# Optimization experiments

Hardware: AMD Instinct MI355X
Metric: run time of the kernel (lower is better)

Reference implementation:

```python
import jax, jax.numpy as jnp
import numpy as np

B, T, I, H = 512, 64, 128, 128
E = I - 1  # encoder_in


def _cell(x, h, c, Wih, Whh, bih, bhh):
    # PyTorch LSTM gate order: i, f, g, o
    g = x @ Wih.T + h @ Whh.T + bih + bhh
    i, f, gg, o = jnp.split(g, 4, axis=-1)
    c2 = jax.nn.sigmoid(f) * c + jax.nn.sigmoid(i) * jnp.tanh(gg)
    h2 = jax.nn.sigmoid(o) * jnp.tanh(c2)
    return h2, c2


def setup_inputs() -> dict:
    key = jax.random.key(0)
    ks = iter(jax.random.split(key, 40))
    n = lambda *s: jax.random.normal(next(ks), s, dtype=jnp.float32) * 0.05
    inp = {
        'input_data': jax.random.normal(next(ks), (B, T, I), dtype=jnp.float32),
        # encoder LSTM (2 layers, input E)
        'enc_Wih0': n(4 * H, E), 'enc_Whh0': n(4 * H, H), 'enc_bih0': n(4 * H), 'enc_bhh0': n(4 * H),
        'enc_Wih1': n(4 * H, H), 'enc_Whh1': n(4 * H, H), 'enc_bih1': n(4 * H), 'enc_bhh1': n(4 * H),
        # decoder LSTM (2 layers, input 1)
        'dec_Wih0': n(4 * H, 1), 'dec_Whh0': n(4 * H, H), 'dec_bih0': n(4 * H), 'dec_bhh0': n(4 * H),
        'dec_Wih1': n(4 * H, H), 'dec_Whh1': n(4 * H, H), 'dec_bih1': n(4 * H), 'dec_bhh1': n(4 * H),
        # input attention MLP: (2H+T)->T->1
        'attn_W1': n(T, 2 * H + T), 'attn_b1': n(T), 'attn_W2': n(1, T), 'attn_b2': n(1),
        # temporal attention MLP: 3H->H->1
        'attnd_W1': n(H, 3 * H), 'attnd_b1': n(H), 'attnd_W2': n(1, H), 'attnd_b2': n(1),
        # decoder input projection (H+1)->1 and output projection 2H->1
        'decin_W': n(1, H + 1), 'decin_b': n(1),
        'proj_W': n(1, 2 * H), 'proj_b': n(1),
    }
    return inp


def reference(input_data, enc_Wih0, enc_Whh0, enc_bih0, enc_bhh0,
              enc_Wih1, enc_Whh1, enc_bih1, enc_bhh1,
              dec_Wih0, dec_Whh0, dec_bih0, dec_bhh0,
              dec_Wih1, dec_Whh1, dec_bih1, dec_bhh1,
              attn_W1, attn_b1, attn_W2, attn_b2,
              attnd_W1, attnd_b1, attnd_W2, attnd_b2,
              decin_W, decin_b, proj_W, proj_b):
    b, t, i = input_data.shape
    e, hdim = i - 1, enc_Whh0.shape[1]
    inp_enc = input_data[:, :, 1:]              # [B,T,E]
    inp_dec = input_data[:, :, 0]               # [B,T]
    inp_perm = jnp.transpose(inp_enc, (0, 2, 1))  # [B,E,T]
    z = jnp.zeros((b, hdim), input_data.dtype)

    def enc_step(carry, x_t):
        h0, c0, h1, c1 = carry
        hc = jnp.concatenate([
            jnp.broadcast_to(h1[:, None, :], (b, e, hdim)),
            jnp.broadcast_to(c1[:, None, :], (b, e, hdim)),
            inp_perm], axis=-1)                              # [B,E,2H+T]
        logits = jnp.tanh(hc @ attn_W1.T + attn_b1) @ attn_W2.T + attn_b2
        a = jax.nn.softmax(logits[..., 0], axis=-1)          # [B,E]
        h0, c0 = _cell(x_t * a, h0, c0, enc_Wih0, enc_Whh0, enc_bih0, enc_bhh0)
        h1, c1 = _cell(h0, h1, c1, enc_Wih1, enc_Whh1, enc_bih1, enc_bhh1)
        return (h0, c0, h1, c1), h1

    _, h_top = jax.lax.scan(enc_step, (z, z, z, z), jnp.transpose(inp_enc, (1, 0, 2)))
    h_exp = jnp.transpose(h_top, (1, 0, 2))  # [B,T,H]

    def dec_step(carry, x_t):
        h0, c0, h1, c1, _ = carry
        hc = jnp.concatenate([
            jnp.broadcast_to(h1[:, None, :], (b, t, hdim)),
            jnp.broadcast_to(c1[:, None, :], (b, t, hdim)),
            h_exp], axis=-1)                                  # [B,T,3H]
        logits = jnp.tanh(hc @ attnd_W1.T + attnd_b1) @ attnd_W2.T + attnd_b2
        a = jax.nn.softmax(logits[..., 0], axis=-1)           # [B,T]
        partial = jnp.einsum('bth,bt->bh', h_exp, a)          # [B,H]
        full = jnp.concatenate([partial, x_t[:, None]], axis=-1)  # [B,H+1]
        din = full @ decin_W.T + decin_b                      # [B,1]
        h0, c0 = _cell(din, h0, c0, dec_Wih0, dec_Whh0, dec_bih0, dec_bhh0)
        h1, c1 = _cell(h0, h1, c1, dec_Wih1, dec_Whh1, dec_bih1, dec_bhh1)
        return (h0, c0, h1, c1, partial), None

    (h0, c0, h1, c1, partial), _ = jax.lax.scan(dec_step, (z, z, z, z, z), jnp.transpose(inp_dec))
    out = jnp.concatenate([h1, partial], axis=-1) @ proj_W.T + proj_b  # [B,1]
    return out
```

## Files before the change

kernel.cpp:

```cpp
#include <hip/hip_runtime.h>

#define BATCH 512
#define TT 64
#define II 128

#define OFF_Wr_e0 0
#define OFF_Wr_e1 (OFF_Wr_e0 + 512*256)
#define OFF_Wr_d1 (OFF_Wr_e1 + 512*256)
#define OFF_bs0e  (OFF_Wr_d1 + 512*256)
#define OFF_bs1e  (OFF_bs0e + 512)
#define OFF_bs0d  (OFF_bs1e + 512)
#define OFF_bs1d  (OFF_bs0d + 512)
#define OFF_xprojT (OFF_bs1d + 512)
#define OFF_hexp   (OFF_xprojT + BATCH*8192)
#define OFF_hprojT (OFF_hexp + BATCH*8192)

struct Params {
  const float* input;
  const float *eWih0, *eWhh0, *ebih0, *ebhh0, *eWih1, *eWhh1, *ebih1, *ebhh1;
  const float *dWih0, *dWhh0, *dbih0, *dbhh0, *dWih1, *dWhh1, *dbih1, *dbhh1;
  const float *aW1, *ab1, *aW2, *ab2;
  const float *adW1, *adb1, *adW2, *adb2;
  const float *dinW, *dinb, *projW, *projb;
  float* ws;
  float* out;
};

#define L2E 1.4426950408889634f

__device__ __forceinline__ float exp2f_(float x){ return __builtin_amdgcn_exp2f(x); }
__device__ __forceinline__ float rcp_(float x){ return __builtin_amdgcn_rcpf(x); }
__device__ __forceinline__ float fast_tanh(float x){
  float t = exp2f_(x * 2.8853900817779268f);
  return 1.f - 2.f * rcp_(t + 1.f);
}
__device__ __forceinline__ float sigm(float x){
  return rcp_(1.f + exp2f_(-x * L2E));
}
__device__ __forceinline__ float wave_max(float v){
  #pragma unroll
  for (int o = 32; o > 0; o >>= 1) v = fmaxf(v, __shfl_xor(v, o, 64));
  return v;
}
__device__ __forceinline__ float wave_sum(float v){
  #pragma unroll
  for (int o = 32; o > 0; o >>= 1) v += __shfl_xor(v, o, 64);
  return v;
}
__device__ __forceinline__ void bar_lds(){
  asm volatile("s_waitcnt lgkmcnt(0)\n\ts_barrier" ::: "memory");
}

#define FMA4(W,V0,V1,V2,V3) \
  a0 += (W).x*(V0).x + (W).y*(V0).y + (W).z*(V0).z + (W).w*(V0).w; \
  a1 += (W).x*(V1).x + (W).y*(V1).y + (W).z*(V1).z + (W).w*(V1).w; \
  a2 += (W).x*(V2).x + (W).y*(V2).y + (W).z*(V2).z + (W).w*(V2).w; \
  a3 += (W).x*(V3).x + (W).y*(V3).y + (W).z*(V3).z + (W).w*(V3).w;

__global__ __launch_bounds__(256) void k_prep(Params p){
  float* ws = p.ws;
  const int gid = blockIdx.x*256 + threadIdx.x;
  const int gsz = gridDim.x*256;
  for (int i = gid; i < 512*256; i += gsz){
    const int j = i >> 8, k = i & 255;
    ws[OFF_Wr_e0 + i] = (k < 128) ? ((k < 127) ? p.eWih0[j*127 + k] : 0.f)
                                  : p.eWhh0[j*128 + (k-128)];
    ws[OFF_Wr_e1 + i] = (k < 128) ? p.eWih1[j*128 + k] : p.eWhh1[j*128 + (k-128)];
    ws[OFF_Wr_d1 + i] = (k < 128) ? p.dWih1[j*128 + k] : p.dWhh1[j*128 + (k-128)];
  }
  for (int i = gid; i < 512; i += gsz){
    ws[OFF_bs0e+i] = p.ebih0[i]+p.ebhh0[i];
    ws[OFF_bs1e+i] = p.ebih1[i]+p.ebhh1[i];
    ws[OFF_bs0d+i] = p.dbih0[i]+p.dbhh0[i];
    ws[OFF_bs1d+i] = p.dbih1[i]+p.dbhh1[i];
  }
}

__global__ __launch_bounds__(256) void k_xproj(Params p){
  __shared__ float xin[64][128];
  __shared__ float w1x[64][64];
  __shared__ float b1s[64];
  const int b = blockIdx.x, tid = threadIdx.x;
  const float* inb = p.input + (size_t)b*(TT*II);
  for (int i = tid; i < 64*128; i += 256){
    const int k = i >> 7, e = i & 127;
    xin[k][e] = (e < 127) ? inb[k*II + 1 + e] : 0.f;
  }
  for (int i = tid; i < 64*64; i += 256){
    const int j = i >> 6, k = i & 63;
    w1x[j][k] = p.aW1[j*320 + 256 + k];
  }
  if (tid < 64) b1s[tid] = p.ab1[tid];
  __syncthreads();
  float* outb = p.ws + OFF_xprojT + (size_t)b*8192;
  for (int i = tid; i < 64*128; i += 256){
    const int j = i >> 7, e = i & 127;
    float acc = b1s[j];
    #pragma unroll 8
    for (int k = 0; k < 64; ++k) acc += xin[k][e] * w1x[j][k];
    outb[i] = acc;
  }
}

__global__ __launch_bounds__(256) void k_hproj(Params p){
  __shared__ float hx[64][129];
  __shared__ float bs[128];
  const int b = blockIdx.x, tid = threadIdx.x;
  const float* hb = p.ws + OFF_hexp + (size_t)b*8192;
  for (int i = tid; i < 64*128; i += 256) hx[i>>7][i&127] = hb[i];
  if (tid < 128) bs[tid] = p.adb1[tid];
  __syncthreads();
  float* outb = p.ws + OFF_hprojT + (size_t)b*8192;
  for (int i = tid; i < 128*64; i += 256){
    const int kk = i >> 6, t2 = i & 63;
    const float* w = p.adW1 + kk*384 + 256;
    float acc = bs[kk];
    #pragma unroll 8
    for (int k = 0; k < 128; ++k) acc += hx[t2][k] * w[k];
    outb[i] = acc;
  }
}

#define ENC_LDS_FLOATS 39776
__global__ __launch_bounds__(1024, 4) void k_enc(Params p){
  extern __shared__ float sm[];
  float* xp   = sm;
  float* Se   = xp + 32768;
  float* c0s  = Se + 2048;
  float* gpA  = c0s + 512;
  float* gpB  = gpA + 2048;
  float* g01s = gpB + 2048;
  float* w2   = g01s + 256;
  float* pm   = w2 + 64;
  float* psu  = pm + 16;
  const int tid = threadIdx.x;
  const int b0 = blockIdx.x*4;
  float* ws = p.ws;

  { const float4* xsrc = (const float4*)(ws + OFF_xprojT + (size_t)b0*8192);
    float4* xdst = (float4*)xp;
    for (int i = tid; i < 8192; i += 1024) xdst[i] = xsrc[i]; }
  for (int i = tid; i < 2048; i += 1024) Se[i] = 0.f;
  if (tid < 512) c0s[tid] = 0.f;
  if (tid < 64) w2[tid] = p.aW2[tid];
  const float b2 = p.ab2[0];

  const int bbW = tid >> 8;
  const int wvq = (tid >> 6) & 3;
  const int kqE = tid & 3, oE = tid >> 2, jjE = oE & 63;
  const int jhE = tid & 1, eE = (tid >> 1) & 127;
  const int jG = tid & 511, khG = tid >> 9;
  const float bias0 = ws[OFF_bs0e + jG];
  const float bias1 = ws[OFF_bs1e + jG];
  const float4* wE1 = (const float4*)(p.aW1 + jjE*320 + kqE*64);
  const float4* wE3 = (const float4*)(ws + OFF_Wr_e0 + (jG<<8) + (khG<<7));
  const float4* wE4 = (const float4*)(ws + OFF_Wr_e1 + (jG<<8) + (khG<<7));
  const float* xrow = p.input + (size_t)(b0+bbW)*8192 + 1 + eE;
  float4 pfE1[4], pfE3[4], pfE4[4];
  #pragma unroll
  for (int i = 0; i < 4; ++i){ pfE1[i]=wE1[i]; pfE3[i]=wE3[i]; pfE4[i]=wE4[i]; }
  __syncthreads();

  for (int t = 0; t < TT; ++t){
    {
      const float4* s1 = (const float4*)(Se + bbW*512 + 256 + kqE*64);
      float a = 0.f;
      #pragma unroll
      for (int kg = 0; kg < 4; ++kg){ float4 w = pfE1[kg], x = s1[kg];
        a += w.x*x.x + w.y*x.y + w.z*x.z + w.w*x.w; }
      #pragma unroll
      for (int kg = 4; kg < 16; ++kg){ float4 w = wE1[kg], x = s1[kg];
        a += w.x*x.x + w.y*x.y + w.z*x.z + w.w*x.w; }
      a += __shfl_xor(a, 1, 64);
      a += __shfl_xor(a, 2, 64);
      if (kqE == 0) g01s[oE] = a;
    }
    bar_lds();
    float accL;
    {
      const float* xpe = xp + bbW*8192 + eE;
      const float* gg = g01s + bbW*64 + jhE*32;
      const float* w2p = w2 + jhE*32;
      float a = 0.f;
      #pragma unroll 8
      for (int q = 0; q < 32; ++q)
        a += w2p[q] * fast_tanh(xpe[(jhE*32+q)*128] + gg[q]);
      a += __shfl_xor(a, 1, 64);
      a += b2;
      if (eE == 127) a = -3.0e38f;
      accL = a;
      const float m = wave_max(a);
      const float pe = exp2f_((a - m)*L2E);
      const float s = wave_sum(pe)*0.5f;
      if ((tid & 63) == 0){ pm[bbW*4+wvq] = m; psu[bbW*4+wvq] = s; }
    }
    bar_lds();
    {
      const float m0=pm[bbW*4],m1=pm[bbW*4+1],m2=pm[bbW*4+2],m3=pm[bbW*4+3];
      const float gm = fmaxf(fmaxf(m0,m1),fmaxf(m2,m3));
      const float tot = psu[bbW*4]*exp2f_((m0-gm)*L2E) + psu[bbW*4+1]*exp2f_((m1-gm)*L2E)
                      + psu[bbW*4+2]*exp2f_((m2-gm)*L2E) + psu[bbW*4+3]*exp2f_((m3-gm)*L2E);
      const float a = exp2f_((accL-gm)*L2E)*rcp_(tot);
      float xv = 0.f;
      if (eE < 127) xv = xrow[t*128] * a;
      Se[bbW*512 + eE] = xv;
    }
    bar_lds();
    {
      float a0,a1,a2,a3; a0=a1=a2=a3 = khG ? 0.f : bias0;
      const float4* x0 = (const float4*)(Se + (khG<<7));
      const float4* x1 = x0 + 128; const float4* x2 = x0 + 256; const float4* x3 = x0 + 384;
      #pragma unroll
      for (int kg = 0; kg < 4; ++kg){ float4 w = pfE3[kg];
        float4 v0=x0[kg],v1=x1[kg],v2=x2[kg],v3=x3[kg]; FMA4(w,v0,v1,v2,v3) }
      #pragma unroll 7
      for (int kg = 4; kg < 32; ++kg){ float4 w = wE3[kg];
        float4 v0=x0[kg],v1=x1[kg],v2=x2[kg],v3=x3[kg]; FMA4(w,v0,v1,v2,v3) }
      float* gp = khG ? gpB : gpA;
      gp[jG]=a0; gp[512+jG]=a1; gp[1024+jG]=a2; gp[1536+jG]=a3;
    }
    bar_lds();
    if (tid < 512){
      const int bb = tid>>7, u = tid&127;
      const float* gA = gpA + bb*512; const float* gB = gpB + bb*512;
      const float gi=gA[u]+gB[u], gf=gA[128+u]+gB[128+u];
      const float gg2=gA[256+u]+gB[256+u], go=gA[384+u]+gB[384+u];
      const float c = sigm(gf)*c0s[tid] + sigm(gi)*fast_tanh(gg2);
      c0s[tid] = c;
      Se[bb*512 + 128 + u] = sigm(go)*fast_tanh(c);
    }
    bar_lds();
    {
      float a0,a1,a2,a3; a0=a1=a2=a3 = khG ? 0.f : bias1;
      const float4* x0 = (const float4*)(Se + 128 + (khG<<7));
      const float4* x1 = x0 + 128; const float4* x2 = x0 + 256; const float4* x3 = x0 + 384;
      #pragma unroll
      for (int kg = 0; kg < 4; ++kg){ float4 w = pfE4[kg];
        float4 v0=x0[kg],v1=x1[kg],v2=x2[kg],v3=x3[kg]; FMA4(w,v0,v1,v2,v3) }
      #pragma unroll 7
      for (int kg = 4; kg < 32; ++kg){ float4 w = wE4[kg];
        float4 v0=x0[kg],v1=x1[kg],v2=x2[kg],v3=x3[kg]; FMA4(w,v0,v1,v2,v3) }
      float* gp = khG ? gpB : gpA;
      gp[jG]=a0; gp[512+jG]=a1; gp[1024+jG]=a2; gp[1536+jG]=a3;
    }
    bar_lds();
    if (tid < 512){
      const int bb = tid>>7, u = tid&127;
      const float* gA = gpA + bb*512; const float* gB = gpB + bb*512;
      const float gi=gA[u]+gB[u], gf=gA[128+u]+gB[128+u];
      const float gg2=gA[256+u]+gB[256+u], go=gA[384+u]+gB[384+u];
      const float c = sigm(gf)*Se[bb*512+384+u] + sigm(gi)*fast_tanh(gg2);
      Se[bb*512+384+u] = c;
      const float h = sigm(go)*fast_tanh(c);
      Se[bb*512+256+u] = h;
      __builtin_nontemporal_store(h, ws + OFF_hexp + (size_t)(b0+bb)*8192 + t*128 + u);
    }
    bar_lds();
  }
}

#define DEC_LDS_FLOATS 40880
__global__ __launch_bounds__(1024, 4) void k_dec(Params p){
  extern __shared__ float sm[];
  float* hp    = sm;
  float* Sd    = hp + 33280;
  float* c0s   = Sd + 1536;
  float* gpA   = c0s + 512;
  float* gpB   = gpA + 2048;
  float* parts = gpB + 2048;
  float* g01d  = parts + 512;
  float* lraw  = g01d + 512;
  float* pm    = lraw + 256;
  float* psu   = pm + 16;
  float* dpart = psu + 16;
  float* wd2   = dpart + 16;
  const int tid = threadIdx.x;
  const int b0 = blockIdx.x*4;
  float* ws = p.ws;

  { const float* hsrc = ws + OFF_hprojT + (size_t)b0*8192;
    for (int i = tid; i < 32768; i += 1024){
      const int bb = i>>13, kk = (i>>6)&127, tl = i&63;
      hp[bb*8320 + kk*65 + tl] = hsrc[i];
    } }
  for (int i = tid; i < 1536; i += 1024) Sd[i] = 0.f;
  if (tid < 512) c0s[tid] = 0.f;
  if (tid < 128) wd2[tid] = p.adW2[tid];
  const float bd2 = p.adb2[0];

  const int bbW = tid >> 8, wvq = (tid >> 6) & 3;
  const int khD = tid & 1, kkD = (tid >> 1) & 127;
  const int kq4 = tid & 3, o4 = tid >> 2, tl4 = o4 & 63;
  const int thC = tid & 1, hC = (tid >> 1) & 127;
  const int jG = tid & 511, khG = tid >> 9;
  const float bias0d = ws[OFF_bs0d + jG];
  const float bias1d = ws[OFF_bs1d + jG];
  const float dW0j = p.dWih0[jG];
  const float dinw_h = p.dinW[hC];
  const float dinw128 = p.dinW[128], dinbv = p.dinb[0];
  const float4* wD1 = (const float4*)(p.adW1 + kkD*384 + khD*128);
  const float4* wD3 = (const float4*)(p.dWhh0 + (jG<<7) + (khG<<6));
  const float4* wD4 = (const float4*)(ws + OFF_Wr_d1 + (jG<<8) + (khG<<7));
  const float* heB = ws + OFF_hexp + (size_t)(b0+bbW)*8192 + thC*4096 + hC;
  float4 pfD1[4], pfD3[4], pfD4[4];
  #pragma unroll
  for (int i = 0; i < 4; ++i){ pfD1[i]=wD1[i]; pfD3[i]=wD3[i]; pfD4[i]=wD4[i]; }
  __syncthreads();

  for (int t = 0; t < TT; ++t){
    {
      const float4* sx = (const float4*)(Sd + bbW*384 + 128 + khD*128);
      float a = 0.f;
      #pragma unroll
      for (int kg = 0; kg < 4; ++kg){ float4 w = pfD1[kg], x = sx[kg];
        a += w.x*x.x + w.y*x.y + w.z*x.z + w.w*x.w; }
      #pragma unroll 7
      for (int kg = 4; kg < 32; ++kg){ float4 w = wD1[kg], x = sx[kg];
        a += w.x*x.x + w.y*x.y + w.z*x.z + w.w*x.w; }
      a += __shfl_xor(a, 1, 64);
      if (khD == 0) g01d[bbW*128 + kkD] = a;
    }
    bar_lds();
    float lacc;
    {
      const float* hpb = hp + bbW*8320 + tl4;
      const float* gg = g01d + bbW*128;
      float a = 0.f;
      #pragma unroll 8
      for (int q = 0; q < 32; ++q){
        const int kk = q*4 + kq4;
        a += wd2[kk] * fast_tanh(hpb[kk*65] + gg[kk]);
      }
      a += __shfl_xor(a, 1, 64);
      a += __shfl_xor(a, 2, 64);
      a += bd2;
      lacc = a;
      if (kq4 == 0) lraw[o4] = a;
      const float m = wave_max(a);
      const float pe = exp2f_((a-m)*L2E);
      const float s = wave_sum(pe)*0.25f;
      if ((tid&63)==0){ pm[bbW*4+wvq]=m; psu[bbW*4+wvq]=s; }
    }
    bar_lds();
    if (tid < 256){
      const int bb = tid>>6;
      const float m0=pm[bb*4],m1=pm[bb*4+1],m2=pm[bb*4+2],m3=pm[bb*4+3];
      const float gm = fmaxf(fmaxf(m0,m1),fmaxf(m2,m3));
      const float tot = psu[bb*4]*exp2f_((m0-gm)*L2E)+psu[bb*4+1]*exp2f_((m1-gm)*L2E)
                      +psu[bb*4+2]*exp2f_((m2-gm)*L2E)+psu[bb*4+3]*exp2f_((m3-gm)*L2E);
      lraw[tid] = exp2f_((lraw[tid]-gm)*L2E)*rcp_(tot);
    }
    bar_lds();
    {
      const float* av = lraw + bbW*64 + thC*32;
      float a = 0.f;
      #pragma unroll 8
      for (int q = 0; q < 32; ++q) a += av[q] * heB[q*128];
      a += __shfl_xor(a, 1, 64);
      if (thC == 0) parts[bbW*128 + hC] = a;
      float v = a * dinw_h;
      v = wave_sum(v)*0.5f;
      if ((tid&63)==0) dpart[bbW*4+wvq] = v;
    }
    bar_lds();
    {
      const float xd0 = p.input[(size_t)(b0+0)*8192 + t*128];
      const float xd1 = p.input[(size_t)(b0+1)*8192 + t*128];
      const float xd2 = p.input[(size_t)(b0+2)*8192 + t*128];
      const float xd3 = p.input[(size_t)(b0+3)*8192 + t*128];
      const float dn0 = dpart[0]+dpart[1]+dpart[2]+dpart[3] + xd0*dinw128 + dinbv;
      const float dn1 = dpart[4]+dpart[5]+dpart[6]+dpart[7] + xd1*dinw128 + dinbv;
      const float dn2 = dpart[8]+dpart[9]+dpart[10]+dpart[11] + xd2*dinw128 + dinbv;
      const float dn3 = dpart[12]+dpart[13]+dpart[14]+dpart[15] + xd3*dinw128 + dinbv;
      float a0,a1,a2,a3;
      if (khG){ a0=a1=a2=a3=0.f; }
      else { a0=bias0d+dn0*dW0j; a1=bias0d+dn1*dW0j; a2=bias0d+dn2*dW0j; a3=bias0d+dn3*dW0j; }
      const float4* x0 = (const float4*)(Sd + (khG<<6));
      const float4* x1 = x0 + 96; const float4* x2 = x0 + 192; const float4* x3 = x0 + 288;
      #pragma unroll
      for (int kg = 0; kg < 4; ++kg){ float4 w = pfD3[kg];
        float4 v0=x0[kg],v1=x1[kg],v2=x2[kg],v3=x3[kg]; FMA4(w,v0,v1,v2,v3) }
      #pragma unroll
      for (int kg = 4; kg < 16; ++kg){ float4 w = wD3[kg];
        float4 v0=x0[kg],v1=x1[kg],v2=x2[kg],v3=x3[kg]; FMA4(w,v0,v1,v2,v3) }
      float* gp = khG ? gpB : gpA;
      gp[jG]=a0; gp[512+jG]=a1; gp[1024+jG]=a2; gp[1536+jG]=a3;
    }
    bar_lds();
    if (tid < 512){
      const int bb = tid>>7, u = tid&127;
      const float* gA = gpA + bb*512; const float* gB = gpB + bb*512;
      const float gi=gA[u]+gB[u], gf=gA[128+u]+gB[128+u];
      const float gg2=gA[256+u]+gB[256+u], go=gA[384+u]+gB[384+u];
      const float c = sigm(gf)*c0s[tid] + sigm(gi)*fast_tanh(gg2);
      c0s[tid] = c;
      Sd[bb*384 + u] = sigm(go)*fast_tanh(c);
    }
    bar_lds();
    {
      float a0,a1,a2,a3; a0=a1=a2=a3 = khG ? 0.f : bias1d;
      const float4* x0 = (const float4*)(Sd + (khG<<7));
      const float4* x1 = x0 + 96; const float4* x2 = x0 + 192; const float4* x3 = x0 + 288;
      #pragma unroll
      for (int kg = 0; kg < 4; ++kg){ float4 w = pfD4[kg];
        float4 v0=x0[kg],v1=x1[kg],v2=x2[kg],v3=x3[kg]; FMA4(w,v0,v1,v2,v3) }
      #pragma unroll 7
      for (int kg = 4; kg < 32; ++kg){ float4 w = wD4[kg];
        float4 v0=x0[kg],v1=x1[kg],v2=x2[kg],v3=x3[kg]; FMA4(w,v0,v1,v2,v3) }
      float* gp = khG ? gpB : gpA;
      gp[jG]=a0; gp[512+jG]=a1; gp[1024+jG]=a2; gp[1536+jG]=a3;
    }
    bar_lds();
    if (tid < 512){
      const int bb = tid>>7, u = tid&127;
      const float* gA = gpA + bb*512; const float* gB = gpB + bb*512;
      const float gi=gA[u]+gB[u], gf=gA[128+u]+gB[128+u];
      const float gg2=gA[256+u]+gB[256+u], go=gA[384+u]+gB[384+u];
      const float c = sigm(gf)*Sd[bb*384+256+u] + sigm(gi)*fast_tanh(gg2);
      Sd[bb*384+256+u] = c;
      Sd[bb*384+128+u] = sigm(go)*fast_tanh(c);
    }
    bar_lds();
  }
  if (tid < 256){
    const int bb = tid>>6, l = tid&63;
    float v = Sd[bb*384+128+l]*p.projW[l] + Sd[bb*384+192+l]*p.projW[64+l]
            + parts[bb*128+l]*p.projW[128+l] + parts[bb*128+64+l]*p.projW[192+l];
    v = wave_sum(v);
    if (l == 0) p.out[b0 + bb] = v + p.projb[0];
  }
}

extern "C" void kernel_launch(void* const* d_in, const int* in_sizes, int n_in,
                              void* d_out, int out_size, void* d_ws, size_t ws_size,
                              hipStream_t stream){
  Params p;
  p.input = (const float*)d_in[0];
  p.eWih0=(const float*)d_in[1];  p.eWhh0=(const float*)d_in[2];
  p.ebih0=(const float*)d_in[3];  p.ebhh0=(const float*)d_in[4];
  p.eWih1=(const float*)d_in[5];  p.eWhh1=(const float*)d_in[6];
  p.ebih1=(const float*)d_in[7];  p.ebhh1=(const float*)d_in[8];
  p.dWih0=(const float*)d_in[9];  p.dWhh0=(const float*)d_in[10];
  p.dbih0=(const float*)d_in[11]; p.dbhh0=(const float*)d_in[12];
  p.dWih1=(const float*)d_in[13]; p.dWhh1=(const float*)d_in[14];
  p.dbih1=(const float*)d_in[15]; p.dbhh1=(const float*)d_in[16];
  p.aW1=(const float*)d_in[17];   p.ab1=(const float*)d_in[18];
  p.aW2=(const float*)d_in[19];   p.ab2=(const float*)d_in[20];
  p.adW1=(const float*)d_in[21];  p.adb1=(const float*)d_in[22];
  p.adW2=(const float*)d_in[23];  p.adb2=(const float*)d_in[24];
  p.dinW=(const float*)d_in[25];  p.dinb=(const float*)d_in[26];
  p.projW=(const float*)d_in[27]; p.projb=(const float*)d_in[28];
  p.ws = (float*)d_ws;
  p.out = (float*)d_out;

  (void)hipFuncSetAttribute(reinterpret_cast<const void*>(k_enc),
      hipFuncAttributeMaxDynamicSharedMemorySize, ENC_LDS_FLOATS*4);
  (void)hipFuncSetAttribute(reinterpret_cast<const void*>(k_dec),
      hipFuncAttributeMaxDynamicSharedMemorySize, DEC_LDS_FLOATS*4);

  hipLaunchKernelGGL(k_prep,  dim3(128), dim3(256), 0, stream, p);
  hipLaunchKernelGGL(k_xproj, dim3(BATCH), dim3(256), 0, stream, p);
  hipLaunchKernelGGL(k_enc,   dim3(128), dim3(1024), ENC_LDS_FLOATS*4, stream, p);
  hipLaunchKernelGGL(k_hproj, dim3(BATCH), dim3(256), 0, stream, p);
  hipLaunchKernelGGL(k_dec,   dim3(128), dim3(1024), DEC_LDS_FLOATS*4, stream, p);
}
```

Before: 5.655 ms.

## Halve recurrent kernel block size and use 4x4 register-tiled gate GEMMs

The encoder and decoder recurrent kernels now run with 512 threads instead of 1024. Each thread computes a 4-gate by 4-batch register tile over a K-slice, and partial sums are reduced with shuffles instead of a two-buffer LDS split-K combine. K-offsets are rotated per lane to spread LDS bank access. Attention loops now cover all of T or E per thread rather than split halves. The weight prefetch-into-register trick and the raw lgkmcnt barrier are dropped in favour of __syncthreads. The aim is fewer threads per barrier and more weight reuse per load, at the cost of more registers per thread and longer serial attention loops.

After: 6.746 ms. 1.19x slower.

```diff
diff --git a/kernel.cpp b/kernel.cpp
--- a/kernel.cpp
+++ b/kernel.cpp
@@ -47,15 +47,20 @@
   for (int o = 32; o > 0; o >>= 1) v += __shfl_xor(v, o, 64);
   return v;
 }
-__device__ __forceinline__ void bar_lds(){
-  asm volatile("s_waitcnt lgkmcnt(0)\n\ts_barrier" ::: "memory");
-}
-
-#define FMA4(W,V0,V1,V2,V3) \
-  a0 += (W).x*(V0).x + (W).y*(V0).y + (W).z*(V0).z + (W).w*(V0).w; \
-  a1 += (W).x*(V1).x + (W).y*(V1).y + (W).z*(V1).z + (W).w*(V1).w; \
-  a2 += (W).x*(V2).x + (W).y*(V2).y + (W).z*(V2).z + (W).w*(V2).w; \
-  a3 += (W).x*(V3).x + (W).y*(V3).y + (W).z*(V3).z + (W).w*(V3).w;
+
+#define DOT(A,W,X) A += (W).x*(X).x + (W).y*(X).y + (W).z*(X).z + (W).w*(X).w;
+#define CMB2(A) A += __shfl_xor(A,1,64); A += __shfl_xor(A,2,64);
+#define CMB3(A) CMB2(A) A += __shfl_xor(A,4,64);
+#define DECL16 float a00=0,a10=0,a20=0,a30=0,a01=0,a11=0,a21=0,a31=0, \
+                     a02=0,a12=0,a22=0,a32=0,a03=0,a13=0,a23=0,a33=0;
+#define GEMM16(WA,WB,WC,WD,XA,XB,XC,XD) \
+  DOT(a00,WA,XA) DOT(a10,WB,XA) DOT(a20,WC,XA) DOT(a30,WD,XA) \
+  DOT(a01,WA,XB) DOT(a11,WB,XB) DOT(a21,WC,XB) DOT(a31,WD,XB) \
+  DOT(a02,WA,XC) DOT(a12,WB,XC) DOT(a22,WC,XC) DOT(a32,WD,XC) \
+  DOT(a03,WA,XD) DOT(a13,WB,XD) DOT(a23,WC,XD) DOT(a33,WD,XD)
+#define CMB2ALL16 CMB2(a00) CMB2(a10) CMB2(a20) CMB2(a30) CMB2(a01) CMB2(a11) \
+  CMB2(a21) CMB2(a31) CMB2(a02) CMB2(a12) CMB2(a22) CMB2(a32) CMB2(a03) \
+  CMB2(a13) CMB2(a23) CMB2(a33)
 
 __global__ __launch_bounds__(256) void k_prep(Params p){
   float* ws = p.ws;
@@ -121,306 +126,344 @@
   }
 }
 
-#define ENC_LDS_FLOATS 39776
-__global__ __launch_bounds__(1024, 4) void k_enc(Params p){
+#define ENC_LDS_FLOATS (32768+2048+512+2048+256+64+8+8)
+__global__ __launch_bounds__(512, 2) void k_enc(Params p){
   extern __shared__ float sm[];
   float* xp   = sm;
   float* Se   = xp + 32768;
   float* c0s  = Se + 2048;
-  float* gpA  = c0s + 512;
-  float* gpB  = gpA + 2048;
-  float* g01s = gpB + 2048;
+  float* gp   = c0s + 512;
+  float* g01s = gp + 2048;
   float* w2   = g01s + 256;
   float* pm   = w2 + 64;
-  float* psu  = pm + 16;
+  float* psu  = pm + 8;
   const int tid = threadIdx.x;
   const int b0 = blockIdx.x*4;
   float* ws = p.ws;
 
   { const float4* xsrc = (const float4*)(ws + OFF_xprojT + (size_t)b0*8192);
     float4* xdst = (float4*)xp;
-    for (int i = tid; i < 8192; i += 1024) xdst[i] = xsrc[i]; }
-  for (int i = tid; i < 2048; i += 1024) Se[i] = 0.f;
-  if (tid < 512) c0s[tid] = 0.f;
+    for (int i = tid; i < 8192; i += 512) xdst[i] = xsrc[i]; }
+  for (int i = tid; i < 2048; i += 512) Se[i] = 0.f;
+  c0s[tid] = 0.f;
   if (tid < 64) w2[tid] = p.aW2[tid];
   const float b2 = p.ab2[0];
 
-  const int bbW = tid >> 8;
-  const int wvq = (tid >> 6) & 3;
-  const int kqE = tid & 3, oE = tid >> 2, jjE = oE & 63;
-  const int jhE = tid & 1, eE = (tid >> 1) & 127;
-  const int jG = tid & 511, khG = tid >> 9;
-  const float bias0 = ws[OFF_bs0e + jG];
-  const float bias1 = ws[OFF_bs1e + jG];
-  const float4* wE1 = (const float4*)(p.aW1 + jjE*320 + kqE*64);
-  const float4* wE3 = (const float4*)(ws + OFF_Wr_e0 + (jG<<8) + (khG<<7));
-  const float4* wE4 = (const float4*)(ws + OFF_Wr_e1 + (jG<<8) + (khG<<7));
-  const float* xrow = p.input + (size_t)(b0+bbW)*8192 + 1 + eE;
-  float4 pfE1[4], pfE3[4], pfE4[4];
-  #pragma unroll
-  for (int i = 0; i < 4; ++i){ pfE1[i]=wE1[i]; pfE3[i]=wE3[i]; pfE4[i]=wE4[i]; }
+  const int kq8 = tid & 7, jjE = tid >> 3;
+  const int k0q8 = kq8 << 5;
+  const int e2 = tid & 127, bb2 = tid >> 7;
+  const int ehalf = (tid >> 6) & 1;
+  const int kq4 = tid & 3, gE = tid >> 2;
+  const int j0 = gE << 2;
+  const int k0q4 = kq4 << 6;
+  const int bbU = tid >> 7, uU = tid & 127;
+
+  const float4 bias0v = *(const float4*)(ws + OFF_bs0e + j0);
+  const float4 bias1v = *(const float4*)(ws + OFF_bs1e + j0);
+  const int offE1 = jjE*320 + k0q8;
+  const int offE3 = OFF_Wr_e0 + j0*256 + k0q4;
+  const int offE4 = OFF_Wr_e1 + j0*256 + k0q4;
   __syncthreads();
 
   for (int t = 0; t < TT; ++t){
     {
-      const float4* s1 = (const float4*)(Se + bbW*512 + 256 + kqE*64);
-      float a = 0.f;
+      float a0=0.f,a1=0.f,a2=0.f,a3=0.f;
       #pragma unroll
-      for (int kg = 0; kg < 4; ++kg){ float4 w = pfE1[kg], x = s1[kg];
-        a += w.x*x.x + w.y*x.y + w.z*x.z + w.w*x.w; }
-      #pragma unroll
-      for (int kg = 4; kg < 16; ++kg){ float4 w = wE1[kg], x = s1[kg];
-        a += w.x*x.x + w.y*x.y + w.z*x.z + w.w*x.w; }
-      a += __shfl_xor(a, 1, 64);
-      a += __shfl_xor(a, 2, 64);
-      if (kqE == 0) g01s[oE] = a;
-    }
-    bar_lds();
+      for (int kg = 0; kg < 8; ++kg){
+        const int idx = (((kg + kq8) & 7) << 2);
+        const float4 w  = *(const float4*)(p.aW1 + offE1 + idx);
+        const float4 v0 = *(const float4*)(Se + 256 + k0q8 + idx);
+        const float4 v1 = *(const float4*)(Se + 768 + k0q8 + idx);
+        const float4 v2 = *(const float4*)(Se + 1280 + k0q8 + idx);
+        const float4 v3 = *(const float4*)(Se + 1792 + k0q8 + idx);
+        DOT(a0,w,v0) DOT(a1,w,v1) DOT(a2,w,v2) DOT(a3,w,v3)
+      }
+      CMB3(a0) CMB3(a1) CMB3(a2) CMB3(a3)
+      if (kq8 == 0){
+        g01s[jjE] = a0; g01s[64+jjE] = a1; g01s[128+jjE] = a2; g01s[192+jjE] = a3;
+      }
+    }
+    __syncthreads();
     float accL;
     {
-      const float* xpe = xp + bbW*8192 + eE;
-      const float* gg = g01s + bbW*64 + jhE*32;
-      const float* w2p = w2 + jhE*32;
-      float a = 0.f;
+      const float* xpe = xp + bb2*8192 + e2;
+      const float* gg = g01s + bb2*64;
+      float a = b2;
       #pragma unroll 8
-      for (int q = 0; q < 32; ++q)
-        a += w2p[q] * fast_tanh(xpe[(jhE*32+q)*128] + gg[q]);
-      a += __shfl_xor(a, 1, 64);
-      a += b2;
-      if (eE == 127) a = -3.0e38f;
+      for (int j = 0; j < 64; ++j)
+        a += w2[j] * fast_tanh(xpe[j*128] + gg[j]);
+      if (e2 == 127) a = -3.0e38f;
       accL = a;
       const float m = wave_max(a);
       const float pe = exp2f_((a - m)*L2E);
-      const float s = wave_sum(pe)*0.5f;
-      if ((tid & 63) == 0){ pm[bbW*4+wvq] = m; psu[bbW*4+wvq] = s; }
-    }
-    bar_lds();
-    {
-      const float m0=pm[bbW*4],m1=pm[bbW*4+1],m2=pm[bbW*4+2],m3=pm[bbW*4+3];
-      const float gm = fmaxf(fmaxf(m0,m1),fmaxf(m2,m3));
-      const float tot = psu[bbW*4]*exp2f_((m0-gm)*L2E) + psu[bbW*4+1]*exp2f_((m1-gm)*L2E)
-                      + psu[bbW*4+2]*exp2f_((m2-gm)*L2E) + psu[bbW*4+3]*exp2f_((m3-gm)*L2E);
-      const float a = exp2f_((accL-gm)*L2E)*rcp_(tot);
+      const float s = wave_sum(pe);
+      if ((tid & 63) == 0){ pm[bb2*2+ehalf] = m; psu[bb2*2+ehalf] = s; }
+    }
+    __syncthreads();
+    {
+      const float m0 = pm[bb2*2], m1 = pm[bb2*2+1];
+      const float gm = fmaxf(m0,m1);
+      const float tot = psu[bb2*2]*exp2f_((m0-gm)*L2E) + psu[bb2*2+1]*exp2f_((m1-gm)*L2E);
+      const float aa = exp2f_((accL-gm)*L2E)*rcp_(tot);
       float xv = 0.f;
-      if (eE < 127) xv = xrow[t*128] * a;
-      Se[bbW*512 + eE] = xv;
-    }
-    bar_lds();
-    {
-      float a0,a1,a2,a3; a0=a1=a2=a3 = khG ? 0.f : bias0;
-      const float4* x0 = (const float4*)(Se + (khG<<7));
-      const float4* x1 = x0 + 128; const float4* x2 = x0 + 256; const float4* x3 = x0 + 384;
-      #pragma unroll
-      for (int kg = 0; kg < 4; ++kg){ float4 w = pfE3[kg];
-        float4 v0=x0[kg],v1=x1[kg],v2=x2[kg],v3=x3[kg]; FMA4(w,v0,v1,v2,v3) }
-      #pragma unroll 7
-      for (int kg = 4; kg < 32; ++kg){ float4 w = wE3[kg];
-        float4 v0=x0[kg],v1=x1[kg],v2=x2[kg],v3=x3[kg]; FMA4(w,v0,v1,v2,v3) }
-      float* gp = khG ? gpB : gpA;
-      gp[jG]=a0; gp[512+jG]=a1; gp[1024+jG]=a2; gp[1536+jG]=a3;
-    }
-    bar_lds();
-    if (tid < 512){
-      const int bb = tid>>7, u = tid&127;
-      const float* gA = gpA + bb*512; const float* gB = gpB + bb*512;
-      const float gi=gA[u]+gB[u], gf=gA[128+u]+gB[128+u];
-      const float gg2=gA[256+u]+gB[256+u], go=gA[384+u]+gB[384+u];
+      if (e2 < 127) xv = p.input[(size_t)(b0+bb2)*8192 + t*128 + 1 + e2] * aa;
+      Se[bb2*512 + e2] = xv;
+    }
+    __syncthreads();
+    {
+      DECL16
+      #pragma unroll 4
+      for (int kg = 0; kg < 16; ++kg){
+        const int idx = (((kg + kq4*2) & 15) << 2);
+        const float4 wA = *(const float4*)(ws + offE3 + idx);
+        const float4 wB = *(const float4*)(ws + offE3 + 256 + idx);
+        const float4 wC = *(const float4*)(ws + offE3 + 512 + idx);
+        const float4 wD = *(const float4*)(ws + offE3 + 768 + idx);
+        const float4 xA = *(const float4*)(Se + k0q4 + idx);
+        const float4 xB = *(const float4*)(Se + 512 + k0q4 + idx);
+        const float4 xC = *(const float4*)(Se + 1024 + k0q4 + idx);
+        const float4 xD = *(const float4*)(Se + 1536 + k0q4 + idx);
+        GEMM16(wA,wB,wC,wD,xA,xB,xC,xD);
+      }
+      CMB2ALL16
+      if (kq4 == 0){
+        *(float4*)(gp + j0)        = make_float4(a00+bias0v.x, a10+bias0v.y, a20+bias0v.z, a30+bias0v.w);
+        *(float4*)(gp + 512 + j0)  = make_float4(a01+bias0v.x, a11+bias0v.y, a21+bias0v.z, a31+bias0v.w);
+        *(float4*)(gp + 1024 + j0) = make_float4(a02+bias0v.x, a12+bias0v.y, a22+bias0v.z, a32+bias0v.w);
+        *(float4*)(gp + 1536 + j0) = make_float4(a03+bias0v.x, a13+bias0v.y, a23+bias0v.z, a33+bias0v.w);
+      }
+    }
+    __syncthreads();
+    {
+      const float* g = gp + bbU*512;
+      const float gi=g[uU], gf=g[128+uU], gg2=g[256+uU], go=g[384+uU];
       const float c = sigm(gf)*c0s[tid] + sigm(gi)*fast_tanh(gg2);
       c0s[tid] = c;
-      Se[bb*512 + 128 + u] = sigm(go)*fast_tanh(c);
-    }
-    bar_lds();
-    {
-      float a0,a1,a2,a3; a0=a1=a2=a3 = khG ? 0.f : bias1;
-      const float4* x0 = (const float4*)(Se + 128 + (khG<<7));
-      const float4* x1 = x0 + 128; const float4* x2 = x0 + 256; const float4* x3 = x0 + 384;
-      #pragma unroll
-      for (int kg = 0; kg < 4; ++kg){ float4 w = pfE4[kg];
-        float4 v0=x0[kg],v1=x1[kg],v2=x2[kg],v3=x3[kg]; FMA4(w,v0,v1,v2,v3) }
-      #pragma unroll 7
-      for (int kg = 4; kg < 32; ++kg){ float4 w = wE4[kg];
-        float4 v0=x0[kg],v1=x1[kg],v2=x2[kg],v3=x3[kg]; FMA4(w,v0,v1,v2,v3) }
-      float* gp = khG ? gpB : gpA;
-      gp[jG]=a0; gp[512+jG]=a1; gp[1024+jG]=a2; gp[1536+jG]=a3;
-    }
-    bar_lds();
-    if (tid < 512){
-      const int bb = tid>>7, u = tid&127;
-      const float* gA = gpA + bb*512; const float* gB = gpB + bb*512;
-      const float gi=gA[u]+gB[u], gf=gA[128+u]+gB[128+u];
-      const float gg2=gA[256+u]+gB[256+u], go=gA[384+u]+gB[384+u];
-      const float c = sigm(gf)*Se[bb*512+384+u] + sigm(gi)*fast_tanh(gg2);
-      Se[bb*512+384+u] = c;
+      Se[bbU*512 + 128 + uU] = sigm(go)*fast_tanh(c);
+    }
+    __syncthreads();
+    {
+      DECL16
+      #pragma unroll 4
+      for (int kg = 0; kg < 16; ++kg){
+        const int idx = (((kg + kq4*2) & 15) << 2);
+        const float4 wA = *(const float4*)(ws + offE4 + idx);
+        const float4 wB = *(const float4*)(ws + offE4 + 256 + idx);
+        const float4 wC = *(const float4*)(ws + offE4 + 512 + idx);
+        const float4 wD = *(const float4*)(ws + offE4 + 768 + idx);
+        const float4 xA = *(const float4*)(Se + 128 + k0q4 + idx);
+        const float4 xB = *(const float4*)(Se + 640 + k0q4 + idx);
+        const float4 xC = *(const float4*)(Se + 1152 + k0q4 + idx);
+        const float4 xD = *(const float4*)(Se + 1664 + k0q4 + idx);
+        GEMM16(wA,wB,wC,wD,xA,xB,xC,xD);
+      }
+      CMB2ALL16
+      if (kq4 == 0){
+        *(float4*)(gp + j0)        = make_float4(a00+bias1v.x, a10+bias1v.y, a20+bias1v.z, a30+bias1v.w);
+        *(float4*)(gp + 512 + j0)  = make_float4(a01+bias1v.x, a11+bias1v.y, a21+bias1v.z, a31+bias1v.w);
+        *(float4*)(gp + 1024 + j0) = make_float4(a02+bias1v.x, a12+bias1v.y, a22+bias1v.z, a32+bias1v.w);
+        *(float4*)(gp + 1536 + j0) = make_float4(a03+bias1v.x, a13+bias1v.y, a23+bias1v.z, a33+bias1v.w);
+      }
+    }
+    __syncthreads();
+    {
+      const float* g = gp + bbU*512;
+      const float gi=g[uU], gf=g[128+uU], gg2=g[256+uU], go=g[384+uU];
+      const float c = sigm(gf)*Se[bbU*512+384+uU] + sigm(gi)*fast_tanh(gg2);
+      Se[bbU*512+384+uU] = c;
       const float h = sigm(go)*fast_tanh(c);
-      Se[bb*512+256+u] = h;
-      __builtin_nontemporal_store(h, ws + OFF_hexp + (size_t)(b0+bb)*8192 + t*128 + u);
-    }
-    bar_lds();
-  }
-}
-
-#define DEC_LDS_FLOATS 40880
-__global__ __launch_bounds__(1024, 4) void k_dec(Params p){
+      Se[bbU*512+256+uU] = h;
+      ws[OFF_hexp + (size_t)(b0+bbU)*8192 + t*128 + uU] = h;
+    }
+    __syncthreads();
+  }
+}
+
+#define DEC_LDS_FLOATS (33280+1536+512+2048+512+256+8+8+8+128+512)
+__global__ __launch_bounds__(512, 2) void k_dec(Params p){
   extern __shared__ float sm[];
   float* hp    = sm;
   float* Sd    = hp + 33280;
   float* c0s   = Sd + 1536;
-  float* gpA   = c0s + 512;
-  float* gpB   = gpA + 2048;
-  float* parts = gpB + 2048;
-  float* g01d  = parts + 512;
+  float* gp    = c0s + 512;
+  float* g01d  = gp + 2048;
   float* lraw  = g01d + 512;
   float* pm    = lraw + 256;
-  float* psu   = pm + 16;
-  float* dpart = psu + 16;
-  float* wd2   = dpart + 16;
+  float* psu   = pm + 8;
+  float* dpart = psu + 8;
+  float* wd2   = dpart + 8;
+  float* parts = wd2 + 128;
   const int tid = threadIdx.x;
   const int b0 = blockIdx.x*4;
   float* ws = p.ws;
 
   { const float* hsrc = ws + OFF_hprojT + (size_t)b0*8192;
-    for (int i = tid; i < 32768; i += 1024){
+    for (int i = tid; i < 32768; i += 512){
       const int bb = i>>13, kk = (i>>6)&127, tl = i&63;
       hp[bb*8320 + kk*65 + tl] = hsrc[i];
     } }
-  for (int i = tid; i < 1536; i += 1024) Sd[i] = 0.f;
-  if (tid < 512) c0s[tid] = 0.f;
+  for (int i = tid; i < 1536; i += 512) Sd[i] = 0.f;
+  c0s[tid] = 0.f;
   if (tid < 128) wd2[tid] = p.adW2[tid];
   const float bd2 = p.adb2[0];
 
-  const int bbW = tid >> 8, wvq = (tid >> 6) & 3;
-  const int khD = tid & 1, kkD = (tid >> 1) & 127;
-  const int kq4 = tid & 3, o4 = tid >> 2, tl4 = o4 & 63;
-  const int thC = tid & 1, hC = (tid >> 1) & 127;
-  const int jG = tid & 511, khG = tid >> 9;
-  const float bias0d = ws[OFF_bs0d + jG];
-  const float bias1d = ws[OFF_bs1d + jG];
-  const float dW0j = p.dWih0[jG];
-  const float dinw_h = p.dinW[hC];
+  const int kq8 = tid & 7, gD1 = tid >> 3;
+  const int kk0 = gD1 << 1, k0d1 = kq8 << 5;
+  const int kqA = tid & 1, tlA = (tid>>1) & 63, bbA = tid >> 7;
+  const int tlh = (tid>>6) & 1;
+  const int hC = tid & 127, bbC = tid >> 7, hh = (tid>>6) & 1;
+  const int kq4 = tid & 3, gG = tid >> 2;
+  const int j0 = gG << 2;
+  const int k0d3 = kq4 << 5, k0d4 = kq4 << 6;
+  const int bbU = tid >> 7, uU = tid & 127;
+
+  const float4 bias0d4 = *(const float4*)(ws + OFF_bs0d + j0);
+  const float4 bias1d4 = *(const float4*)(ws + OFF_bs1d + j0);
+  const float4 dW0v = *(const float4*)(p.dWih0 + j0);
+  const int offD1 = kk0*384 + k0d1;
+  const int offD3 = j0*128 + k0d3;
+  const int offD4 = OFF_Wr_d1 + j0*256 + k0d4;
+  const int heBase = OFF_hexp + (b0+bbC)*8192 + hC;
+  const float wdin_h = p.dinW[hC];
   const float dinw128 = p.dinW[128], dinbv = p.dinb[0];
-  const float4* wD1 = (const float4*)(p.adW1 + kkD*384 + khD*128);
-  const float4* wD3 = (const float4*)(p.dWhh0 + (jG<<7) + (khG<<6));
-  const float4* wD4 = (const float4*)(ws + OFF_Wr_d1 + (jG<<8) + (khG<<7));
-  const float* heB = ws + OFF_hexp + (size_t)(b0+bbW)*8192 + thC*4096 + hC;
-  float4 pfD1[4], pfD3[4], pfD4[4];
-  #pragma unroll
-  for (int i = 0; i < 4; ++i){ pfD1[i]=wD1[i]; pfD3[i]=wD3[i]; pfD4[i]=wD4[i]; }
   __syncthreads();
 
   for (int t = 0; t < TT; ++t){
     {
-      const float4* sx = (const float4*)(Sd + bbW*384 + 128 + khD*128);
-      float a = 0.f;
+      float a00=0,a01=0,a02=0,a03=0,a10=0,a11=0,a12=0,a13=0;
       #pragma unroll
-      for (int kg = 0; kg < 4; ++kg){ float4 w = pfD1[kg], x = sx[kg];
-        a += w.x*x.x + w.y*x.y + w.z*x.z + w.w*x.w; }
-      #pragma unroll 7
-      for (int kg = 4; kg < 32; ++kg){ float4 w = wD1[kg], x = sx[kg];
-        a += w.x*x.x + w.y*x.y + w.z*x.z + w.w*x.w; }
-      a += __shfl_xor(a, 1, 64);
-      if (khD == 0) g01d[bbW*128 + kkD] = a;
-    }
-    bar_lds();
-    float lacc;
-    {
-      const float* hpb = hp + bbW*8320 + tl4;
-      const float* gg = g01d + bbW*128;
+      for (int kg = 0; kg < 8; ++kg){
+        const int idx = (((kg + kq8) & 7) << 2);
+        const float4 w0 = *(const float4*)(p.adW1 + offD1 + idx);
+        const float4 w1 = *(const float4*)(p.adW1 + offD1 + 384 + idx);
+        const float4 x0 = *(const float4*)(Sd + 128 + k0d1 + idx);
+        const float4 x1 = *(const float4*)(Sd + 512 + k0d1 + idx);
+        const float4 x2 = *(const float4*)(Sd + 896 + k0d1 + idx);
+        const float4 x3 = *(const float4*)(Sd + 1280 + k0d1 + idx);
+        DOT(a00,w0,x0) DOT(a01,w0,x1) DOT(a02,w0,x2) DOT(a03,w0,x3)
+        DOT(a10,w1,x0) DOT(a11,w1,x1) DOT(a12,w1,x2) DOT(a13,w1,x3)
+      }
+      CMB3(a00) CMB3(a01) CMB3(a02) CMB3(a03)
+      CMB3(a10) CMB3(a11) CMB3(a12) CMB3(a13)
+      if (kq8 == 0){
+        g01d[kk0] = a00;       g01d[kk0+1] = a10;
+        g01d[128+kk0] = a01;   g01d[128+kk0+1] = a11;
+        g01d[256+kk0] = a02;   g01d[256+kk0+1] = a12;
+        g01d[384+kk0] = a03;   g01d[384+kk0+1] = a13;
+      }
+    }
+    __syncthreads();
+    {
+      const float* hpb = hp + bbA*8320 + tlA;
+      const float* gg = g01d + bbA*128;
       float a = 0.f;
       #pragma unroll 8
-      for (int q = 0; q < 32; ++q){
-        const int kk = q*4 + kq4;
+      for (int q = 0; q < 64; ++q){
+        const int kk = kqA*64 + q;
         a += wd2[kk] * fast_tanh(hpb[kk*65] + gg[kk]);
       }
       a += __shfl_xor(a, 1, 64);
-      a += __shfl_xor(a, 2, 64);
       a += bd2;
-      lacc = a;
-      if (kq4 == 0) lraw[o4] = a;
       const float m = wave_max(a);
       const float pe = exp2f_((a-m)*L2E);
-      const float s = wave_sum(pe)*0.25f;
-      if ((tid&63)==0){ pm[bbW*4+wvq]=m; psu[bbW*4+wvq]=s; }
-    }
-    bar_lds();
+      const float s = wave_sum(pe)*0.5f;
+      if ((tid & 63) == 0){ pm[bbA*2+tlh] = m; psu[bbA*2+tlh] = s; }
+      if (kqA == 0) lraw[bbA*64 + tlA] = a;
+    }
+    __syncthreads();
     if (tid < 256){
-      const int bb = tid>>6;
-      const float m0=pm[bb*4],m1=pm[bb*4+1],m2=pm[bb*4+2],m3=pm[bb*4+3];
-      const float gm = fmaxf(fmaxf(m0,m1),fmaxf(m2,m3));
-      const float tot = psu[bb*4]*exp2f_((m0-gm)*L2E)+psu[bb*4+1]*exp2f_((m1-gm)*L2E)
-                      +psu[bb*4+2]*exp2f_((m2-gm)*L2E)+psu[bb*4+3]*exp2f_((m3-gm)*L2E);
+      const int bb = tid >> 6;
+      const float m0 = pm[bb*2], m1 = pm[bb*2+1];
+      const float gm = fmaxf(m0,m1);
+      const float tot = psu[bb*2]*exp2f_((m0-gm)*L2E) + psu[bb*2+1]*exp2f_((m1-gm)*L2E);
       lraw[tid] = exp2f_((lraw[tid]-gm)*L2E)*rcp_(tot);
     }
-    bar_lds();
-    {
-      const float* av = lraw + bbW*64 + thC*32;
+    __syncthreads();
+    {
+      const float* he = ws + heBase;
+      const float* av = lraw + bbC*64;
       float a = 0.f;
       #pragma unroll 8
-      for (int q = 0; q < 32; ++q) a += av[q] * heB[q*128];
-      a += __shfl_xor(a, 1, 64);
-      if (thC == 0) parts[bbW*128 + hC] = a;
-      float v = a * dinw_h;
-      v = wave_sum(v)*0.5f;
-      if ((tid&63)==0) dpart[bbW*4+wvq] = v;
-    }
-    bar_lds();
+      for (int t2 = 0; t2 < 64; ++t2)
+        a += av[t2] * he[t2*128];
+      parts[bbC*128 + hC] = a;
+      float v = a * wdin_h;
+      v = wave_sum(v);
+      if ((tid & 63) == 0) dpart[bbC*2+hh] = v;
+    }
+    __syncthreads();
     {
       const float xd0 = p.input[(size_t)(b0+0)*8192 + t*128];
       const float xd1 = p.input[(size_t)(b0+1)*8192 + t*128];
       const float xd2 = p.input[(size_t)(b0+2)*8192 + t*128];
       const float xd3 = p.input[(size_t)(b0+3)*8192 + t*128];
-      const float dn0 = dpart[0]+dpart[1]+dpart[2]+dpart[3] + xd0*dinw128 + dinbv;
-      const float dn1 = dpart[4]+dpart[5]+dpart[6]+dpart[7] + xd1*dinw128 + dinbv;
-      const float dn2 = dpart[8]+dpart[9]+dpart[10]+dpart[11] + xd2*dinw128 + dinbv;
-      const float dn3 = dpart[12]+dpart[13]+dpart[14]+dpart[15] + xd3*dinw128 + dinbv;
-      float a0,a1,a2,a3;
-      if (khG){ a0=a1=a2=a3=0.f; }
-      else { a0=bias0d+dn0*dW0j; a1=bias0d+dn1*dW0j; a2=bias0d+dn2*dW0j; a3=bias0d+dn3*dW0j; }
-      const float4* x0 = (const float4*)(Sd + (khG<<6));
-      const float4* x1 = x0 + 96; const float4* x2 = x0 + 192; const float4* x3 = x0 + 288;
+      const float dn0 = dpart[0]+dpart[1] + xd0*dinw128 + dinbv;
+      const float dn1 = dpart[2]+dpart[3] + xd1*dinw128 + dinbv;
+      const float dn2 = dpart[4]+dpart[5] + xd2*dinw128 + dinbv;
+      const float dn3 = dpart[6]+dpart[7] + xd3*dinw128 + dinbv;
+      DECL16
       #pragma unroll
-      for (int kg = 0; kg < 4; ++kg){ float4 w = pfD3[kg];
-        float4 v0=x0[kg],v1=x1[kg],v2=x2[kg],v3=x3[kg]; FMA4(w,v0,v1,v2,v3) }
-      #pragma unroll
-      for (int kg = 4; kg < 16; ++kg){ float4 w = wD3[kg];
-        float4 v0=x0[kg],v1=x1[kg],v2=x2[kg],v3=x3[kg]; FMA4(w,v0,v1,v2,v3) }
-      float* gp = khG ? gpB : gpA;
-      gp[jG]=a0; gp[512+jG]=a1; gp[1024+jG]=a2; gp[1536+jG]=a3;
-    }
-    bar_lds();
-    if (tid < 512){
-      const int bb = tid>>7, u = tid&127;
-      const float* gA = gpA + bb*512; const float* gB = gpB + bb*512;
-      const float gi=gA[u]+gB[u], gf=gA[128+u]+gB[128+u];
-      const float gg2=gA[256+u]+gB[256+u], go=gA[384+u]+gB[384+u];
+      for (int kg = 0; kg < 8; ++kg){
+        const int idx = (((kg + kq4*2) & 7) << 2);
+        const float4 wA = *(const float4*)(p.dWhh0 + offD3 + idx);
+        const float4 wB = *(const float4*)(p.dWhh0 + offD3 + 128 + idx);
+        const float4 wC = *(const float4*)(p.dWhh0 + offD3 + 256 + idx);
+        const float4 wD = *(const float4*)(p.dWhh0 + offD3 + 384 + idx);
+        const float4 xA = *(const float4*)(Sd + k0d3 + idx);
+        const float4 xB = *(const float4*)(Sd + 384 + k0d3 + idx);
+        const float4 xC = *(const float4*)(Sd + 768 + k0d3 + idx);
+        const float4 xD = *(const float4*)(Sd + 1152 + k0d3 + idx);
+        GEMM16(wA,wB,wC,wD,xA,xB,xC,xD);
+      }
+      CMB2ALL16
+      if (kq4 == 0){
+        *(float4*)(gp + j0)        = make_float4(a00+bias0d4.x+dn0*dW0v.x, a10+bias0d4.y+dn0*dW0v.y, a20+bias0d4.z+dn0*dW0v.z, a30+bias0d4.w+dn0*dW0v.w);
+        *(float4*)(gp + 512 + j0)  = make_float4(a01+bias0d4.x+dn1*dW0v.x, a11+bias0d4.y+dn1*dW0v.y, a21+bias0d4.z+dn1*dW0v.z, a31+bias0d4.w+dn1*dW0v.w);
+        *(float4*)(gp + 1024 + j0) = make_float4(a02+bias0d4.x+dn2*dW0v.x, a12+bias0d4.y+dn2*dW0v.y, a22+bias0d4.z+dn2*dW0v.z, a32+bias0d4.w+dn2*dW0v.w);
+        *(float4*)(gp + 1536 + j0) = make_float4(a03+bias0d4.x+dn3*dW0v.x, a13+bias0d4.y+dn3*dW0v.y, a23+bias0d4.z+dn3*dW0v.z, a33+bias0d4.w+dn3*dW0v.w);
+      }
+    }
+    __syncthreads();
+    {
+      const float* g = gp + bbU*512;
+      const float gi=g[uU], gf=g[128+uU], gg2=g[256+uU], go=g[384+uU];
       const float c = sigm(gf)*c0s[tid] + sigm(gi)*fast_tanh(gg2);
       c0s[tid] = c;
-      Sd[bb*384 + u] = sigm(go)*fast_tanh(c);
-    }
-    bar_lds();
-    {
-      float a0,a1,a2,a3; a0=a1=a2=a3 = khG ? 0.f : bias1d;
-      const float4* x0 = (const float4*)(Sd + (khG<<7));
-      const float4* x1 = x0 + 96; const float4* x2 = x0 + 192; const float4* x3 = x0 + 288;
-      #pragma unroll
-      for (int kg = 0; kg < 4; ++kg){ float4 w = pfD4[kg];
-        float4 v0=x0[kg],v1=x1[kg],v2=x2[kg],v3=x3[kg]; FMA4(w,v0,v1,v2,v3) }
-      #pragma unroll 7
-      for (int kg = 4; kg < 32; ++kg){ float4 w = wD4[kg];
-        float4 v0=x0[kg],v1=x1[kg],v2=x2[kg],v3=x3[kg]; FMA4(w,v0,v1,v2,v3) }
-      float* gp = khG ? gpB : gpA;
-      gp[jG]=a0; gp[512+jG]=a1; gp[1024+jG]=a2; gp[1536+jG]=a3;
-    }
-    bar_lds();
-    if (tid < 512){
-      const int bb = tid>>7, u = tid&127;
-      const float* gA = gpA + bb*512; const float* gB = gpB + bb*512;
-      const float gi=gA[u]+gB[u], gf=gA[128+u]+gB[128+u];
-      const float gg2=gA[256+u]+gB[256+u], go=gA[384+u]+gB[384+u];
-      const float c = sigm(gf)*Sd[bb*384+256+u] + sigm(gi)*fast_tanh(gg2);
-      Sd[bb*384+256+u] = c;
-      Sd[bb*384+128+u] = sigm(go)*fast_tanh(c);
-    }
-    bar_lds();
+      Sd[bbU*384 + uU] = sigm(go)*fast_tanh(c);
+    }
+    __syncthreads();
+    {
+      DECL16
+      #pragma unroll 4
+      for (int kg = 0; kg < 16; ++kg){
+        const int idx = (((kg + kq4*2) & 15) << 2);
+        const float4 wA = *(const float4*)(ws + offD4 + idx);
+        const float4 wB = *(const float4*)(ws + offD4 + 256 + idx);
+        const float4 wC = *(const float4*)(ws + offD4 + 512 + idx);
+        const float4 wD = *(const float4*)(ws + offD4 + 768 + idx);
+        const float4 xA = *(const float4*)(Sd + k0d4 + idx);
+        const float4 xB = *(const float4*)(Sd + 384 + k0d4 + idx);
+        const float4 xC = *(const float4*)(Sd + 768 + k0d4 + idx);
+        const float4 xD = *(const float4*)(Sd + 1152 + k0d4 + idx);
+        GEMM16(wA,wB,wC,wD,xA,xB,xC,xD);
+      }
+      CMB2ALL16
+      if (kq4 == 0){
+        *(float4*)(gp + j0)        = make_float4(a00+bias1d4.x, a10+bias1d4.y, a20+bias1d4.z, a30+bias1d4.w);
+        *(float4*)(gp + 512 + j0)  = make_float4(a01+bias1d4.x, a11+bias1d4.y, a21+bias1d4.z, a31+bias1d4.w);
+        *(float4*)(gp + 1024 + j0) = make_float4(a02+bias1d4.x, a12+bias1d4.y, a22+bias1d4.z, a32+bias1d4.w);
+        *(float4*)(gp + 1536 + j0) = make_float4(a03+bias1d4.x, a13+bias1d4.y, a23+bias1d4.z, a33+bias1d4.w);
+      }
+    }
+    __syncthreads();
+    {
+      const float* g = gp + bbU*512;
+      const float gi=g[uU], gf=g[128+uU], gg2=g[256+uU], go=g[384+uU];
+      const float c = sigm(gf)*Sd[bbU*384+256+uU] + sigm(gi)*fast_tanh(gg2);
+      Sd[bbU*384+256+uU] = c;
+      Sd[bbU*384+128+uU] = sigm(go)*fast_tanh(c);
+    }
+    __syncthreads();
   }
   if (tid < 256){
     const int bb = tid>>6, l = tid&63;
@@ -460,7 +503,7 @@
 
   hipLaunchKernelGGL(k_prep,  dim3(128), dim3(256), 0, stream, p);
   hipLaunchKernelGGL(k_xproj, dim3(BATCH), dim3(256), 0, stream, p);
-  hipLaunchKernelGGL(k_enc,   dim3(128), dim3(1024), ENC_LDS_FLOATS*4, stream, p);
+  hipLaunchKernelGGL(k_enc,   dim3(128), dim3(512), ENC_LDS_FLOATS*4, stream, p);
   hipLaunchKernelGGL(k_hproj, dim3(BATCH), dim3(256), 0, stream, p);
-  hipLaunchKernelGGL(k_dec,   dim3(128), dim3(1024), DEC_LDS_FLOATS*4, stream, p);
-}
+  hipLaunchKernelGGL(k_dec,   dim3(128), dim3(512), DEC_LDS_FLOATS*4, stream, p);
+}
```
